# Kernel tuning notes

Hardware: AMD Instinct MI355X
Metric: run time of the kernel (lower is better)

## Reference

```python
import jax, jax.numpy as jnp
import numpy as np

N_NODES, N_EDGES, DIM, N_LAYERS, N_GRAPHS, N_CLASSES = 50000, 640000, 128, 5, 512, 128


def setup_inputs() -> dict:
    key = jax.random.key(0)
    ks = jax.random.split(key, 10)
    x = jnp.zeros((N_NODES,), dtype=jnp.int32)  # Embedding(1, D) -> all indices 0
    edge_index = jax.random.randint(ks[0], (2, N_EDGES), 0, N_NODES, dtype=jnp.int32)
    edge_attr = jax.random.normal(ks[1], (N_EDGES, DIM), dtype=jnp.float32)
    batch = jnp.sort(jax.random.randint(ks[2], (N_NODES,), 0, N_GRAPHS, dtype=jnp.int32))
    s = 1.0 / np.sqrt(DIM)
    node_emb = jax.random.normal(ks[3], (1, DIM), dtype=jnp.float32)
    Ws = jax.random.normal(ks[4], (N_LAYERS, DIM, DIM), dtype=jnp.float32) * s
    bs = jnp.zeros((N_LAYERS, DIM), dtype=jnp.float32)
    Wes = jax.random.normal(ks[5], (N_LAYERS, DIM, DIM), dtype=jnp.float32) * s
    Wp = jax.random.normal(ks[6], (DIM, N_CLASSES), dtype=jnp.float32) * s
    bp = jnp.zeros((N_CLASSES,), dtype=jnp.float32)
    return {"x": x, "edge_index": edge_index, "edge_attr": edge_attr, "batch": batch,
            "node_emb": node_emb, "Ws": Ws, "bs": bs, "Wes": Wes, "Wp": Wp, "bp": bp}


def reference(x, edge_index, edge_attr, batch, node_emb, Ws, bs, Wes, Wp, bp):
    src, dst = edge_index[0], edge_index[1]
    h = node_emb[x]  # [N, D] embedding lookup (vocab=1)
    n = h.shape[0]
    e = src.shape[0]
    deg = jax.ops.segment_sum(jnp.ones((e,), h.dtype), dst, num_segments=n)
    deg = jnp.maximum(deg, 1.0)[:, None]  # mean aggregation denominator
    for l in range(N_LAYERS):
        hw = h @ Ws[l] + bs[l]                       # [N, D]
        msg = hw[src] + edge_attr @ Wes[l]           # [E, D] gather + edge transform
        agg = jax.ops.segment_sum(msg, dst, num_segments=n) / deg  # scatter-mean
        h = agg + hw                                 # root connection
        if l < N_LAYERS - 1:
            h = jax.nn.relu(h)                       # relu on all but last layer
        # dropout is identity in eval mode
    g = N_GRAPHS
    cnt = jnp.maximum(jax.ops.segment_sum(jnp.ones((n,), h.dtype), batch, num_segments=g), 1.0)
    pooled = jax.ops.segment_sum(h, batch, num_segments=g) / cnt[:, None]  # global_mean_pool
    return pooled @ Wp + bp  # [G, num_clases]
```

## Files before the change

kernel.cpp:

```cpp
#include <hip/hip_runtime.h>

#define N_NODES   50000
#define N_EDGES   640000
#define DIM       128
#define N_LAYERS  5
#define N_GRAPHS  512
#define N_CLASSES 128
#define NB_SCAN   196

typedef __attribute__((ext_vector_type(8))) short short8;
typedef __attribute__((ext_vector_type(4))) float floatx4;

__device__ inline float bfhi(unsigned u) { return __uint_as_float(u & 0xffff0000u); }
__device__ inline float bflo(unsigned u) { return __uint_as_float(u << 16); }
__device__ inline unsigned f2bf(float f) {
  unsigned x = __float_as_uint(f);
  return (x + 0x7fffu + ((x >> 16) & 1u)) >> 16;
}

__global__ void k_zero(int* __restrict__ deg, int* __restrict__ fill,
                       float* __restrict__ pool, float* __restrict__ cnt) {
  int i = blockIdx.x * 256 + threadIdx.x;
  if (i < N_NODES) { deg[i] = 0; fill[i] = 0; }
  if (i < N_GRAPHS * DIM) pool[i] = 0.f;
  if (i < N_GRAPHS) cnt[i] = 0.f;
}

__global__ void k_deg(const int* __restrict__ dst, int* __restrict__ deg) {
  int e = blockIdx.x * 256 + threadIdx.x;
  if (e < N_EDGES) atomicAdd(&deg[dst[e]], 1);
}

__global__ void k_scan1(const int* __restrict__ deg, int* __restrict__ bsum) {
  __shared__ int s[256];
  int t = threadIdx.x, i = blockIdx.x * 256 + t;
  s[t] = (i < N_NODES) ? deg[i] : 0;
  __syncthreads();
  for (int o = 128; o > 0; o >>= 1) {
    if (t < o) s[t] += s[t + o];
    __syncthreads();
  }
  if (t == 0) bsum[blockIdx.x] = s[0];
}

__global__ void k_scan2(int* __restrict__ bsum) {
  __shared__ int s[256];
  int t = threadIdx.x;
  s[t] = (t < NB_SCAN) ? bsum[t] : 0;
  __syncthreads();
  for (int o = 1; o < 256; o <<= 1) {
    int add = (t >= o) ? s[t - o] : 0;
    __syncthreads();
    s[t] += add;
    __syncthreads();
  }
  int ex = (t == 0) ? 0 : s[t - 1];
  if (t < NB_SCAN) bsum[t] = ex;
}

__global__ void k_scan3(const int* __restrict__ deg, const int* __restrict__ bsum,
                        int* __restrict__ row_ptr) {
  __shared__ int s[256];
  int t = threadIdx.x, i = blockIdx.x * 256 + t;
  s[t] = (i < N_NODES) ? deg[i] : 0;
  __syncthreads();
  for (int o = 1; o < 256; o <<= 1) {
    int add = (t >= o) ? s[t - o] : 0;
    __syncthreads();
    s[t] += add;
    __syncthreads();
  }
  int ex = bsum[blockIdx.x] + ((t == 0) ? 0 : s[t - 1]);
  if (i < N_NODES) row_ptr[i] = ex;
  if (blockIdx.x == 0 && t == 0) row_ptr[N_NODES] = N_EDGES;
}

__global__ void k_fill(const int* __restrict__ src, const int* __restrict__ dst,
                       const int* __restrict__ row_ptr, int* __restrict__ fill,
                       int2* __restrict__ col) {
  int e = blockIdx.x * 256 + threadIdx.x;
  if (e < N_EDGES) {
    int d = dst[e];
    int pos = row_ptr[d] + atomicAdd(&fill[d], 1);
    col[pos] = make_int2(src[e], e);
  }
}

__global__ void k_wconv(const float* __restrict__ Ws, const float* __restrict__ Wes,
                        unsigned short* __restrict__ Wt_s, unsigned short* __restrict__ Wt_e) {
  int idx = blockIdx.x * 256 + threadIdx.x;
  int which = idx / (N_LAYERS * DIM * DIM);
  int rem = idx - which * (N_LAYERS * DIM * DIM);
  int l = rem >> 14;
  int c = (rem >> 7) & 127;
  int k = rem & 127;
  const float* W = which ? Wes : Ws;
  unsigned short* O = which ? Wt_e : Wt_s;
  float v = W[((size_t)l * DIM + k) * DIM + c];
  O[((size_t)l * DIM + c) * DIM + k] = (unsigned short)f2bf(v);
}

__global__ void k_v0(const float* __restrict__ node_emb, const float* __restrict__ Ws0,
                     float* __restrict__ v0) {
  int c = threadIdx.x;
  float acc = 0.f;
  for (int k = 0; k < DIM; k++) acc += node_emb[k] * Ws0[(size_t)k * DIM + c];
  v0[c] = acc;
}

__global__ void k_ean_init(const int* __restrict__ row_ptr, const int2* __restrict__ col,
                           const float* __restrict__ edge_attr,
                           unsigned short* __restrict__ ean, float* __restrict__ rdeg) {
  int sub = threadIdx.x >> 5;
  int lane = threadIdx.x & 31;
  int i = blockIdx.x * 8 + sub;
  if (i >= N_NODES) return;
  int b = row_ptr[i], e = row_ptr[i + 1];
  float ax = 0.f, ay = 0.f, az = 0.f, aw = 0.f;
  int p = b;
  for (; p + 4 <= e; p += 4) {
    int e0 = col[p].y, e1 = col[p + 1].y, e2 = col[p + 2].y, e3 = col[p + 3].y;
    float4 v0 = ((const float4*)(edge_attr + (size_t)e0 * DIM))[lane];
    float4 v1 = ((const float4*)(edge_attr + (size_t)e1 * DIM))[lane];
    float4 v2 = ((const float4*)(edge_attr + (size_t)e2 * DIM))[lane];
    float4 v3 = ((const float4*)(edge_attr + (size_t)e3 * DIM))[lane];
    ax += v0.x + v1.x + v2.x + v3.x;
    ay += v0.y + v1.y + v2.y + v3.y;
    az += v0.z + v1.z + v2.z + v3.z;
    aw += v0.w + v1.w + v2.w + v3.w;
  }
  for (; p < e; p++) {
    int e0 = col[p].y;
    float4 v0 = ((const float4*)(edge_attr + (size_t)e0 * DIM))[lane];
    ax += v0.x; ay += v0.y; az += v0.z; aw += v0.w;
  }
  float r = 1.0f / (float)max(e - b, 1);
  if (lane == 0) rdeg[i] = r;
  uint2 o;
  o.x = f2bf(ax * r) | (f2bf(ay * r) << 16);
  o.y = f2bf(az * r) | (f2bf(aw * r) << 16);
  ((uint2*)(ean + (size_t)i * DIM))[lane] = o;
}

__global__ __launch_bounds__(256) void k_gemm0(
    const unsigned short* __restrict__ ean, const unsigned short* __restrict__ W1,
    const float* __restrict__ v0, const float* __restrict__ bias,
    const int* __restrict__ deg, unsigned short* __restrict__ hout) {
  __shared__ unsigned short sW[128][72];
  int tid = threadIdx.x;
  int wave = tid >> 6, lane = tid & 63;
  int quad = lane >> 4, l16 = lane & 15;
  int row0 = blockIdx.x * 64;
  int row_a = row0 + wave * 16 + l16;
  floatx4 acc[8];
  #pragma unroll
  for (int ci = 0; ci < 8; ci++) acc[ci] = (floatx4){0.f, 0.f, 0.f, 0.f};

  for (int kc = 0; kc < 128; kc += 64) {
    __syncthreads();
    #pragma unroll
    for (int q = 0; q < 4; q++) {
      int s = tid + 256 * q;
      int r = s >> 3, seg = s & 7;
      *(uint4*)(&sW[r][seg * 8]) =
          *(const uint4*)(W1 + (size_t)r * DIM + kc + seg * 8);
    }
    __syncthreads();
    #pragma unroll
    for (int ks = 0; ks < 64; ks += 32) {
      short8 a = {0, 0, 0, 0, 0, 0, 0, 0};
      if (row_a < N_NODES)
        a = *(const short8*)(ean + (size_t)row_a * DIM + kc + ks + quad * 8);
      #pragma unroll
      for (int ci = 0; ci < 8; ci++) {
        short8 b = *(const short8*)(&sW[ci * 16 + l16][ks + quad * 8]);
        acc[ci] = __builtin_amdgcn_mfma_f32_16x16x32_bf16(a, b, acc[ci], 0, 0, 0);
      }
    }
  }
  #pragma unroll
  for (int ci = 0; ci < 8; ci++) {
    int col = ci * 16 + l16;
    float bv = bias[col];
    float vv = v0[col];
    #pragma unroll
    for (int r = 0; r < 4; r++) {
      int row = row0 + wave * 16 + quad * 4 + r;
      if (row < N_NODES) {
        float s = (deg[row] > 0) ? 2.f : 1.f;
        float v = acc[ci][r] + bv + s * vv;
        v = fmaxf(v, 0.f);
        hout[(size_t)row * DIM + col] = (unsigned short)f2bf(v);
      }
    }
  }
}

#define ACC8(v) { a0 += bflo(v.x); a1 += bfhi(v.x); a2 += bflo(v.y); a3 += bfhi(v.y); \
                  a4 += bflo(v.z); a5 += bfhi(v.z); a6 += bflo(v.w); a7 += bfhi(v.w); }

__global__ __launch_bounds__(256) void k_layer(
    const int* __restrict__ row_ptr, const int2* __restrict__ col,
    const unsigned short* __restrict__ hin, const float* __restrict__ rdeg,
    const unsigned short* __restrict__ ean,
    const unsigned short* __restrict__ W0, const unsigned short* __restrict__ W1,
    const float* __restrict__ bias, unsigned short* __restrict__ hout, int relu) {
  __shared__ unsigned short sU[64][136];
  __shared__ unsigned short sW[128][72];
  int tid = threadIdx.x;
  int row0 = blockIdx.x * 64;

  {
    int g = tid >> 4, glane = tid & 15;
    for (int n = 0; n < 4; n++) {
      int r = g + n * 16;
      int i = row0 + r;
      if (i < N_NODES) {
        int b = row_ptr[i], e = row_ptr[i + 1];
        float a0 = 0.f, a1 = 0.f, a2 = 0.f, a3 = 0.f,
              a4 = 0.f, a5 = 0.f, a6 = 0.f, a7 = 0.f;
        int p = b;
        for (; p + 4 <= e; p += 4) {
          int j0 = col[p].x, j1 = col[p + 1].x, j2 = col[p + 2].x, j3 = col[p + 3].x;
          uint4 w0 = *(const uint4*)(hin + (size_t)j0 * DIM + glane * 8);
          uint4 w1 = *(const uint4*)(hin + (size_t)j1 * DIM + glane * 8);
          uint4 w2 = *(const uint4*)(hin + (size_t)j2 * DIM + glane * 8);
          uint4 w3 = *(const uint4*)(hin + (size_t)j3 * DIM + glane * 8);
          ACC8(w0); ACC8(w1); ACC8(w2); ACC8(w3);
        }
        for (; p < e; p++) {
          int j0 = col[p].x;
          uint4 w0 = *(const uint4*)(hin + (size_t)j0 * DIM + glane * 8);
          ACC8(w0);
        }
        float rr = rdeg[i];
        uint4 hv = *(const uint4*)(hin + (size_t)i * DIM + glane * 8);
        uint4 o;
        o.x = f2bf(bflo(hv.x) + a0 * rr) | (f2bf(bfhi(hv.x) + a1 * rr) << 16);
        o.y = f2bf(bflo(hv.y) + a2 * rr) | (f2bf(bfhi(hv.y) + a3 * rr) << 16);
        o.z = f2bf(bflo(hv.z) + a4 * rr) | (f2bf(bfhi(hv.z) + a5 * rr) << 16);
        o.w = f2bf(bflo(hv.w) + a6 * rr) | (f2bf(bfhi(hv.w) + a7 * rr) << 16);
        *(uint4*)(&sU[r][glane * 8]) = o;
      } else {
        *(uint4*)(&sU[r][glane * 8]) = make_uint4(0u, 0u, 0u, 0u);
      }
    }
  }

  int wave = tid >> 6, lane = tid & 63;
  int quad = lane >> 4, l16 = lane & 15;
  int row_a = row0 + wave * 16 + l16;
  floatx4 acc[8];
  #pragma unroll
  for (int ci = 0; ci < 8; ci++) acc[ci] = (floatx4){0.f, 0.f, 0.f, 0.f};

  for (int m = 0; m < 2; m++) {
    const unsigned short* W = m ? W1 : W0;
    for (int kc = 0; kc < 128; kc += 64) {
      __syncthreads();
      #pragma unroll
      for (int q = 0; q < 4; q++) {
        int s = tid + 256 * q;
        int r = s >> 3, seg = s & 7;
        *(uint4*)(&sW[r][seg * 8]) =
            *(const uint4*)(W + (size_t)r * DIM + kc + seg * 8);
      }
      __syncthreads();
      #pragma unroll
      for (int ks = 0; ks < 64; ks += 32) {
        short8 a;
        if (m == 0) {
          a = *(const short8*)(&sU[wave * 16 + l16][kc + ks + quad * 8]);
        } else {
          a = (short8){0, 0, 0, 0, 0, 0, 0, 0};
          if (row_a < N_NODES)
            a = *(const short8*)(ean + (size_t)row_a * DIM + kc + ks + quad * 8);
        }
        #pragma unroll
        for (int ci = 0; ci < 8; ci++) {
          short8 b = *(const short8*)(&sW[ci * 16 + l16][ks + quad * 8]);
          acc[ci] = __builtin_amdgcn_mfma_f32_16x16x32_bf16(a, b, acc[ci], 0, 0, 0);
        }
      }
    }
  }
  #pragma unroll
  for (int ci = 0; ci < 8; ci++) {
    int col_ = ci * 16 + l16;
    float bv = bias[col_];
    #pragma unroll
    for (int r = 0; r < 4; r++) {
      int row = row0 + wave * 16 + quad * 4 + r;
      if (row < N_NODES) {
        float v = acc[ci][r] + bv;
        if (relu) v = fmaxf(v, 0.f);
        hout[(size_t)row * DIM + col_] = (unsigned short)f2bf(v);
      }
    }
  }
}

__global__ void k_pool(const unsigned short* __restrict__ h, const int* __restrict__ batch,
                       float* __restrict__ pool, float* __restrict__ cnt) {
  int t = threadIdx.x;
  int i0 = blockIdx.x * 128;
  int iend = min(i0 + 128, N_NODES);
  float acc = 0.f;
  int cur = -1, run = 0;
  for (int i = i0; i < iend; i++) {
    int g = batch[i];
    if (g != cur) {
      if (cur >= 0) {
        atomicAdd(&pool[(size_t)cur * DIM + t], acc);
        if (t == 0) atomicAdd(&cnt[cur], (float)run);
      }
      acc = 0.f; run = 0; cur = g;
    }
    acc += __uint_as_float(((unsigned)h[(size_t)i * DIM + t]) << 16);
    run++;
  }
  if (cur >= 0) {
    atomicAdd(&pool[(size_t)cur * DIM + t], acc);
    if (t == 0) atomicAdd(&cnt[cur], (float)run);
  }
}

__global__ void k_out(const float* __restrict__ pool, const float* __restrict__ cnt,
                      const float* __restrict__ Wp, const float* __restrict__ bp,
                      float* __restrict__ out) {
  __shared__ float sp[DIM];
  int g = blockIdx.x, t = threadIdx.x;
  sp[t] = pool[(size_t)g * DIM + t];
  __syncthreads();
  float r = 1.0f / fmaxf(cnt[g], 1.0f);
  float acc = 0.f;
  for (int k = 0; k < DIM; k++) acc += sp[k] * Wp[(size_t)k * N_CLASSES + t];
  out[(size_t)g * N_CLASSES + t] = acc * r + bp[t];
}

extern "C" void kernel_launch(void* const* d_in, const int* in_sizes, int n_in,
                              void* d_out, int out_size, void* d_ws, size_t ws_size,
                              hipStream_t stream) {
  (void)in_sizes; (void)n_in; (void)out_size; (void)ws_size;
  const int*   x          = (const int*)d_in[0];
  const int*   edge_index = (const int*)d_in[1];
  const float* edge_attr  = (const float*)d_in[2];
  const int*   batch      = (const int*)d_in[3];
  const float* node_emb   = (const float*)d_in[4];
  const float* Ws         = (const float*)d_in[5];
  const float* bsin       = (const float*)d_in[6];
  const float* Wes        = (const float*)d_in[7];
  const float* Wp         = (const float*)d_in[8];
  const float* bp         = (const float*)d_in[9];
  (void)x;
  float* out = (float*)d_out;
  const int* src = edge_index;
  const int* dst = edge_index + N_EDGES;

  char* p = (char*)d_ws;
  auto alloc = [&](size_t bytes) {
    void* q = (void*)p;
    p += (bytes + 255) & ~(size_t)255;
    return q;
  };
  unsigned short* h    = (unsigned short*)alloc((size_t)N_NODES * DIM * 2);
  unsigned short* h2   = (unsigned short*)alloc((size_t)N_NODES * DIM * 2);
  unsigned short* ean  = (unsigned short*)alloc((size_t)N_NODES * DIM * 2);
  unsigned short* Wt_s = (unsigned short*)alloc((size_t)N_LAYERS * DIM * DIM * 2);
  unsigned short* Wt_e = (unsigned short*)alloc((size_t)N_LAYERS * DIM * DIM * 2);
  int*   deg     = (int*)  alloc((size_t)N_NODES * 4);
  float* rdeg    = (float*)alloc((size_t)N_NODES * 4);
  int*   row_ptr = (int*)  alloc((size_t)(N_NODES + 64) * 4);
  int*   fill    = (int*)  alloc((size_t)N_NODES * 4);
  int2*  col     = (int2*) alloc((size_t)N_EDGES * 8);
  float* pool    = (float*)alloc((size_t)N_GRAPHS * DIM * 4);
  float* cnt     = (float*)alloc((size_t)N_GRAPHS * 4);
  int*   bsum    = (int*)  alloc(256 * 4);
  float* v0      = (float*)alloc(DIM * 4);

  k_zero<<<256, 256, 0, stream>>>(deg, fill, pool, cnt);
  k_deg<<<(N_EDGES + 255) / 256, 256, 0, stream>>>(dst, deg);
  k_scan1<<<NB_SCAN, 256, 0, stream>>>(deg, bsum);
  k_scan2<<<1, 256, 0, stream>>>(bsum);
  k_scan3<<<NB_SCAN, 256, 0, stream>>>(deg, bsum, row_ptr);
  k_fill<<<(N_EDGES + 255) / 256, 256, 0, stream>>>(src, dst, row_ptr, fill, col);
  k_wconv<<<(2 * N_LAYERS * DIM * DIM) / 256, 256, 0, stream>>>(Ws, Wes, Wt_s, Wt_e);
  k_v0<<<1, DIM, 0, stream>>>(node_emb, Ws, v0);
  k_ean_init<<<(N_NODES + 7) / 8, 256, 0, stream>>>(row_ptr, col, edge_attr, ean, rdeg);

  k_gemm0<<<(N_NODES + 63) / 64, 256, 0, stream>>>(
      ean, Wt_e, v0, bsin, deg, h);
  const unsigned short* hin = h;
  unsigned short* hout = h2;
  for (int l = 1; l < N_LAYERS; l++) {
    k_layer<<<(N_NODES + 63) / 64, 256, 0, stream>>>(
        row_ptr, col, hin, rdeg, ean,
        Wt_s + (size_t)l * DIM * DIM, Wt_e + (size_t)l * DIM * DIM,
        bsin + (size_t)l * DIM, hout, (l < N_LAYERS - 1) ? 1 : 0);
    const unsigned short* tmp = hout; hout = (unsigned short*)hin; hin = tmp;
  }
  k_pool<<<(N_NODES + 127) / 128, 128, 0, stream>>>(h, batch, pool, cnt);
  k_out<<<N_GRAPHS, N_CLASSES, 0, stream>>>(pool, cnt, Wp, bp, out);
}
```

Baseline: 758.0 us.

## Fuse pooling into last layer, edge-parallel LDS-atomic aggregation, merge small kernels

The neighbour gather in each layer is now edge-parallel. Each edge locates its destination row with a binary search over a shared row_ptr slice, then adds into an fp32 shared accumulator with LDS atomics. The previous per-row loop let threads with high-degree rows stall the others. The root term is combined when the MFMA A-fragment is built, the first weight tile is staged before the gather, and the final layer atomically adds its outputs into the pooled buffer, which removes k_pool. Graph counts are folded into k_deg and the v0 computation into k_wconv, saving launches; the costs are many LDS atomics and global atomics on pool.

```diff
diff --git a/kernel.cpp b/kernel.cpp
--- a/kernel.cpp
+++ b/kernel.cpp
@@ -19,16 +19,18 @@
 }
 
 __global__ void k_zero(int* __restrict__ deg, int* __restrict__ fill,
-                       float* __restrict__ pool, float* __restrict__ cnt) {
+                       float* __restrict__ pool, int* __restrict__ cntI) {
   int i = blockIdx.x * 256 + threadIdx.x;
   if (i < N_NODES) { deg[i] = 0; fill[i] = 0; }
   if (i < N_GRAPHS * DIM) pool[i] = 0.f;
-  if (i < N_GRAPHS) cnt[i] = 0.f;
-}
-
-__global__ void k_deg(const int* __restrict__ dst, int* __restrict__ deg) {
+  if (i < N_GRAPHS) cntI[i] = 0;
+}
+
+__global__ void k_deg(const int* __restrict__ dst, int* __restrict__ deg,
+                      const int* __restrict__ batch, int* __restrict__ cntI) {
   int e = blockIdx.x * 256 + threadIdx.x;
   if (e < N_EDGES) atomicAdd(&deg[dst[e]], 1);
+  if (e < N_NODES) atomicAdd(&cntI[batch[e]], 1);
 }
 
 __global__ void k_scan1(const int* __restrict__ deg, int* __restrict__ bsum) {
@@ -87,7 +89,17 @@
 }
 
 __global__ void k_wconv(const float* __restrict__ Ws, const float* __restrict__ Wes,
-                        unsigned short* __restrict__ Wt_s, unsigned short* __restrict__ Wt_e) {
+                        unsigned short* __restrict__ Wt_s, unsigned short* __restrict__ Wt_e,
+                        const float* __restrict__ node_emb, float* __restrict__ v0) {
+  if (blockIdx.x == 640) {
+    int c = threadIdx.x;
+    if (c < DIM) {
+      float acc = 0.f;
+      for (int k = 0; k < DIM; k++) acc += node_emb[k] * Ws[(size_t)k * DIM + c];
+      v0[c] = acc;
+    }
+    return;
+  }
   int idx = blockIdx.x * 256 + threadIdx.x;
   int which = idx / (N_LAYERS * DIM * DIM);
   int rem = idx - which * (N_LAYERS * DIM * DIM);
@@ -98,14 +110,6 @@
   unsigned short* O = which ? Wt_e : Wt_s;
   float v = W[((size_t)l * DIM + k) * DIM + c];
   O[((size_t)l * DIM + c) * DIM + k] = (unsigned short)f2bf(v);
-}
-
-__global__ void k_v0(const float* __restrict__ node_emb, const float* __restrict__ Ws0,
-                     float* __restrict__ v0) {
-  int c = threadIdx.x;
-  float acc = 0.f;
-  for (int k = 0; k < DIM; k++) acc += node_emb[k] * Ws0[(size_t)k * DIM + c];
-  v0[c] = acc;
 }
 
 __global__ void k_ean_init(const int* __restrict__ row_ptr, const int2* __restrict__ col,
@@ -196,143 +200,135 @@
   }
 }
 
-#define ACC8(v) { a0 += bflo(v.x); a1 += bfhi(v.x); a2 += bflo(v.y); a3 += bfhi(v.y); \
-                  a4 += bflo(v.z); a5 += bfhi(v.z); a6 += bflo(v.w); a7 += bfhi(v.w); }
-
 __global__ __launch_bounds__(256) void k_layer(
     const int* __restrict__ row_ptr, const int2* __restrict__ col,
     const unsigned short* __restrict__ hin, const float* __restrict__ rdeg,
     const unsigned short* __restrict__ ean,
     const unsigned short* __restrict__ W0, const unsigned short* __restrict__ W1,
-    const float* __restrict__ bias, unsigned short* __restrict__ hout, int relu) {
-  __shared__ unsigned short sU[64][136];
+    const float* __restrict__ bias, unsigned short* __restrict__ hout,
+    const int* __restrict__ batch, float* __restrict__ pool, int relu) {
+  __shared__ float sAcc[64][132];
   __shared__ unsigned short sW[128][72];
+  __shared__ int srp[65];
+  __shared__ int sbatch[64];
   int tid = threadIdx.x;
   int row0 = blockIdx.x * 64;
 
+  #pragma unroll
+  for (int q = 0; q < 4; q++) {
+    int s = tid + 256 * q;
+    int r = s >> 3, seg = s & 7;
+    *(uint4*)(&sW[r][seg * 8]) = *(const uint4*)(W0 + (size_t)r * DIM + seg * 8);
+  }
+  for (int z = tid; z < 64 * 132; z += 256) ((float*)sAcc)[z] = 0.f;
+  if (tid <= 64) srp[tid] = row_ptr[min(row0 + tid, N_NODES)];
+  if (tid < 64) sbatch[tid] = (row0 + tid < N_NODES) ? batch[row0 + tid] : 0;
+  __syncthreads();
+
   {
     int g = tid >> 4, glane = tid & 15;
-    for (int n = 0; n < 4; n++) {
-      int r = g + n * 16;
-      int i = row0 + r;
-      if (i < N_NODES) {
-        int b = row_ptr[i], e = row_ptr[i + 1];
-        float a0 = 0.f, a1 = 0.f, a2 = 0.f, a3 = 0.f,
-              a4 = 0.f, a5 = 0.f, a6 = 0.f, a7 = 0.f;
-        int p = b;
-        for (; p + 4 <= e; p += 4) {
-          int j0 = col[p].x, j1 = col[p + 1].x, j2 = col[p + 2].x, j3 = col[p + 3].x;
-          uint4 w0 = *(const uint4*)(hin + (size_t)j0 * DIM + glane * 8);
-          uint4 w1 = *(const uint4*)(hin + (size_t)j1 * DIM + glane * 8);
-          uint4 w2 = *(const uint4*)(hin + (size_t)j2 * DIM + glane * 8);
-          uint4 w3 = *(const uint4*)(hin + (size_t)j3 * DIM + glane * 8);
-          ACC8(w0); ACC8(w1); ACC8(w2); ACC8(w3);
-        }
-        for (; p < e; p++) {
-          int j0 = col[p].x;
-          uint4 w0 = *(const uint4*)(hin + (size_t)j0 * DIM + glane * 8);
-          ACC8(w0);
-        }
-        float rr = rdeg[i];
-        uint4 hv = *(const uint4*)(hin + (size_t)i * DIM + glane * 8);
-        uint4 o;
-        o.x = f2bf(bflo(hv.x) + a0 * rr) | (f2bf(bfhi(hv.x) + a1 * rr) << 16);
-        o.y = f2bf(bflo(hv.y) + a2 * rr) | (f2bf(bfhi(hv.y) + a3 * rr) << 16);
-        o.z = f2bf(bflo(hv.z) + a4 * rr) | (f2bf(bfhi(hv.z) + a5 * rr) << 16);
-        o.w = f2bf(bflo(hv.w) + a6 * rr) | (f2bf(bfhi(hv.w) + a7 * rr) << 16);
-        *(uint4*)(&sU[r][glane * 8]) = o;
-      } else {
-        *(uint4*)(&sU[r][glane * 8]) = make_uint4(0u, 0u, 0u, 0u);
-      }
-    }
-  }
+    int base = srp[0], end = srp[64];
+    for (int p = base + g; p < end; p += 16) {
+      int s = col[p].x;
+      int i = 0;
+      #pragma unroll
+      for (int st = 32; st >= 1; st >>= 1)
+        if (srp[i + st] <= p) i += st;
+      uint4 hv = *(const uint4*)(hin + (size_t)s * DIM + glane * 8);
+      float* a = &sAcc[i][glane * 8];
+      atomicAdd(&a[0], bflo(hv.x)); atomicAdd(&a[1], bfhi(hv.x));
+      atomicAdd(&a[2], bflo(hv.y)); atomicAdd(&a[3], bfhi(hv.y));
+      atomicAdd(&a[4], bflo(hv.z)); atomicAdd(&a[5], bfhi(hv.z));
+      atomicAdd(&a[6], bflo(hv.w)); atomicAdd(&a[7], bfhi(hv.w));
+    }
+  }
+  __syncthreads();
 
   int wave = tid >> 6, lane = tid & 63;
   int quad = lane >> 4, l16 = lane & 15;
-  int row_a = row0 + wave * 16 + l16;
+  int ra = wave * 16 + l16;
+  int row_a = row0 + ra;
+  float rr = (row_a < N_NODES) ? rdeg[row_a] : 0.f;
   floatx4 acc[8];
   #pragma unroll
   for (int ci = 0; ci < 8; ci++) acc[ci] = (floatx4){0.f, 0.f, 0.f, 0.f};
 
-  for (int m = 0; m < 2; m++) {
-    const unsigned short* W = m ? W1 : W0;
-    for (int kc = 0; kc < 128; kc += 64) {
-      __syncthreads();
+  auto build_u = [&](int cb) -> short8 {
+    short8 a = {0, 0, 0, 0, 0, 0, 0, 0};
+    if (row_a < N_NODES) {
+      uint4 hv = *(const uint4*)(hin + (size_t)row_a * DIM + cb);
+      const float* s = &sAcc[ra][cb];
+      unsigned u0 = f2bf(bflo(hv.x) + s[0] * rr), u1 = f2bf(bfhi(hv.x) + s[1] * rr);
+      unsigned u2 = f2bf(bflo(hv.y) + s[2] * rr), u3 = f2bf(bfhi(hv.y) + s[3] * rr);
+      unsigned u4 = f2bf(bflo(hv.z) + s[4] * rr), u5 = f2bf(bfhi(hv.z) + s[5] * rr);
+      unsigned u6 = f2bf(bflo(hv.w) + s[6] * rr), u7 = f2bf(bfhi(hv.w) + s[7] * rr);
+      a = (short8){(short)u0, (short)u1, (short)u2, (short)u3,
+                   (short)u4, (short)u5, (short)u6, (short)u7};
+    }
+    return a;
+  };
+  auto stage = [&](const unsigned short* W, int kc) {
+    #pragma unroll
+    for (int q = 0; q < 4; q++) {
+      int s = tid + 256 * q;
+      int r = s >> 3, seg = s & 7;
+      *(uint4*)(&sW[r][seg * 8]) = *(const uint4*)(W + (size_t)r * DIM + kc + seg * 8);
+    }
+  };
+  auto mfma_chunk = [&](int m, int kc) {
+    #pragma unroll
+    for (int ks = 0; ks < 64; ks += 32) {
+      int cb = kc + ks + quad * 8;
+      short8 a;
+      if (m == 0) {
+        a = build_u(cb);
+      } else {
+        a = (short8){0, 0, 0, 0, 0, 0, 0, 0};
+        if (row_a < N_NODES)
+          a = *(const short8*)(ean + (size_t)row_a * DIM + cb);
+      }
       #pragma unroll
-      for (int q = 0; q < 4; q++) {
-        int s = tid + 256 * q;
-        int r = s >> 3, seg = s & 7;
-        *(uint4*)(&sW[r][seg * 8]) =
-            *(const uint4*)(W + (size_t)r * DIM + kc + seg * 8);
-      }
-      __syncthreads();
-      #pragma unroll
-      for (int ks = 0; ks < 64; ks += 32) {
-        short8 a;
-        if (m == 0) {
-          a = *(const short8*)(&sU[wave * 16 + l16][kc + ks + quad * 8]);
-        } else {
-          a = (short8){0, 0, 0, 0, 0, 0, 0, 0};
-          if (row_a < N_NODES)
-            a = *(const short8*)(ean + (size_t)row_a * DIM + kc + ks + quad * 8);
-        }
-        #pragma unroll
-        for (int ci = 0; ci < 8; ci++) {
-          short8 b = *(const short8*)(&sW[ci * 16 + l16][ks + quad * 8]);
-          acc[ci] = __builtin_amdgcn_mfma_f32_16x16x32_bf16(a, b, acc[ci], 0, 0, 0);
-        }
-      }
-    }
-  }
+      for (int ci = 0; ci < 8; ci++) {
+        short8 b = *(const short8*)(&sW[ci * 16 + l16][ks + quad * 8]);
+        acc[ci] = __builtin_amdgcn_mfma_f32_16x16x32_bf16(a, b, acc[ci], 0, 0, 0);
+      }
+    }
+  };
+
+  mfma_chunk(0, 0);
+  __syncthreads(); stage(W0, 64); __syncthreads(); mfma_chunk(0, 64);
+  __syncthreads(); stage(W1, 0);  __syncthreads(); mfma_chunk(1, 0);
+  __syncthreads(); stage(W1, 64); __syncthreads(); mfma_chunk(1, 64);
+
   #pragma unroll
   for (int ci = 0; ci < 8; ci++) {
     int col_ = ci * 16 + l16;
     float bv = bias[col_];
     #pragma unroll
     for (int r = 0; r < 4; r++) {
-      int row = row0 + wave * 16 + quad * 4 + r;
+      int rt = wave * 16 + quad * 4 + r;
+      int row = row0 + rt;
       if (row < N_NODES) {
         float v = acc[ci][r] + bv;
-        if (relu) v = fmaxf(v, 0.f);
-        hout[(size_t)row * DIM + col_] = (unsigned short)f2bf(v);
-      }
-    }
-  }
-}
-
-__global__ void k_pool(const unsigned short* __restrict__ h, const int* __restrict__ batch,
-                       float* __restrict__ pool, float* __restrict__ cnt) {
-  int t = threadIdx.x;
-  int i0 = blockIdx.x * 128;
-  int iend = min(i0 + 128, N_NODES);
-  float acc = 0.f;
-  int cur = -1, run = 0;
-  for (int i = i0; i < iend; i++) {
-    int g = batch[i];
-    if (g != cur) {
-      if (cur >= 0) {
-        atomicAdd(&pool[(size_t)cur * DIM + t], acc);
-        if (t == 0) atomicAdd(&cnt[cur], (float)run);
-      }
-      acc = 0.f; run = 0; cur = g;
-    }
-    acc += __uint_as_float(((unsigned)h[(size_t)i * DIM + t]) << 16);
-    run++;
-  }
-  if (cur >= 0) {
-    atomicAdd(&pool[(size_t)cur * DIM + t], acc);
-    if (t == 0) atomicAdd(&cnt[cur], (float)run);
-  }
-}
-
-__global__ void k_out(const float* __restrict__ pool, const float* __restrict__ cnt,
+        if (relu) {
+          v = fmaxf(v, 0.f);
+          hout[(size_t)row * DIM + col_] = (unsigned short)f2bf(v);
+        } else {
+          atomicAdd(&pool[(size_t)sbatch[rt] * DIM + col_], v);
+        }
+      }
+    }
+  }
+}
+
+__global__ void k_out(const float* __restrict__ pool, const int* __restrict__ cntI,
                       const float* __restrict__ Wp, const float* __restrict__ bp,
                       float* __restrict__ out) {
   __shared__ float sp[DIM];
   int g = blockIdx.x, t = threadIdx.x;
   sp[t] = pool[(size_t)g * DIM + t];
   __syncthreads();
-  float r = 1.0f / fmaxf(cnt[g], 1.0f);
+  float r = 1.0f / fmaxf((float)cntI[g], 1.0f);
   float acc = 0.f;
   for (int k = 0; k < DIM; k++) acc += sp[k] * Wp[(size_t)k * N_CLASSES + t];
   out[(size_t)g * N_CLASSES + t] = acc * r + bp[t];
@@ -374,18 +370,17 @@
   int*   fill    = (int*)  alloc((size_t)N_NODES * 4);
   int2*  col     = (int2*) alloc((size_t)N_EDGES * 8);
   float* pool    = (float*)alloc((size_t)N_GRAPHS * DIM * 4);
-  float* cnt     = (float*)alloc((size_t)N_GRAPHS * 4);
+  int*   cntI    = (int*)  alloc((size_t)N_GRAPHS * 4);
   int*   bsum    = (int*)  alloc(256 * 4);
   float* v0      = (float*)alloc(DIM * 4);
 
-  k_zero<<<256, 256, 0, stream>>>(deg, fill, pool, cnt);
-  k_deg<<<(N_EDGES + 255) / 256, 256, 0, stream>>>(dst, deg);
+  k_zero<<<256, 256, 0, stream>>>(deg, fill, pool, cntI);
+  k_deg<<<(N_EDGES + 255) / 256, 256, 0, stream>>>(dst, deg, batch, cntI);
   k_scan1<<<NB_SCAN, 256, 0, stream>>>(deg, bsum);
   k_scan2<<<1, 256, 0, stream>>>(bsum);
   k_scan3<<<NB_SCAN, 256, 0, stream>>>(deg, bsum, row_ptr);
   k_fill<<<(N_EDGES + 255) / 256, 256, 0, stream>>>(src, dst, row_ptr, fill, col);
-  k_wconv<<<(2 * N_LAYERS * DIM * DIM) / 256, 256, 0, stream>>>(Ws, Wes, Wt_s, Wt_e);
-  k_v0<<<1, DIM, 0, stream>>>(node_emb, Ws, v0);
+  k_wconv<<<641, 256, 0, stream>>>(Ws, Wes, Wt_s, Wt_e, node_emb, v0);
   k_ean_init<<<(N_NODES + 7) / 8, 256, 0, stream>>>(row_ptr, col, edge_attr, ean, rdeg);
 
   k_gemm0<<<(N_NODES + 63) / 64, 256, 0, stream>>>(
@@ -396,9 +391,8 @@
     k_layer<<<(N_NODES + 63) / 64, 256, 0, stream>>>(
         row_ptr, col, hin, rdeg, ean,
         Wt_s + (size_t)l * DIM * DIM, Wt_e + (size_t)l * DIM * DIM,
-        bsin + (size_t)l * DIM, hout, (l < N_LAYERS - 1) ? 1 : 0);
+        bsin + (size_t)l * DIM, hout, batch, pool, (l < N_LAYERS - 1) ? 1 : 0);
     const unsigned short* tmp = hout; hout = (unsigned short*)hin; hin = tmp;
   }
-  k_pool<<<(N_NODES + 127) / 128, 128, 0, stream>>>(h, batch, pool, cnt);
-  k_out<<<N_GRAPHS, N_CLASSES, 0, stream>>>(pool, cnt, Wp, bp, out);
-}
+  k_out<<<N_GRAPHS, N_CLASSES, 0, stream>>>(pool, cntI, Wp, bp, out);
+}
```

After: 2.832 ms. 3.74x slower.
